# Performance work log

Measured on AMD Instinct MI355X. Metric: run time of the kernel, lower is better.

Reference implementation:

```python
import jax, jax.numpy as jnp
import numpy as np

N = 50000      # nodes
E = 800000     # edges (before self-loops)
G = 128        # graphs in batch
IN = 128       # input_dim
H = 4          # heads
D = 32         # hidden_dim per head (H*D = 128)
L = 3          # n_layers
COND = 7       # data.stats features
LAT = 32       # latent_dim
NEG_SLOPE = 0.2


def setup_inputs() -> dict:
    key = jax.random.key(0)
    ks = jax.random.split(key, 10)
    s = 0.1
    return {
        "x": jax.random.normal(ks[0], (N, IN), jnp.float32),
        "cond": jax.random.normal(ks[1], (G, COND), jnp.float32),
        "W": jax.random.normal(ks[2], (L, IN, H * D), jnp.float32) * s,
        "a_src": jax.random.normal(ks[3], (L, H, D), jnp.float32) * s,
        "a_dst": jax.random.normal(ks[4], (L, H, D), jnp.float32) * s,
        "conv_bias": jnp.zeros((L, H * D), jnp.float32),
        "bn_gamma": jnp.ones((H * D + COND,), jnp.float32),
        "bn_beta": jnp.zeros((H * D + COND,), jnp.float32),
        "fc_w": jax.random.normal(ks[5], (H * D + COND, LAT), jnp.float32) * s,
        "fc_b": jnp.zeros((LAT,), jnp.float32),
        "edge_index": jax.random.randint(ks[6], (2, E), 0, N, jnp.int32),
        "batch": jnp.sort(jax.random.randint(ks[7], (N,), 0, G, jnp.int32)),
    }


def _leaky(x, slope):
    return jnp.where(x > 0, x, slope * x)


def _gat_layer(x, W, a_s, a_d, b, src, dst):
    # x: [N, F_in] -> h: [N, H, D]
    h = (x @ W).reshape(N, H, D)
    al_s = jnp.einsum("nhd,hd->nh", h, a_s)   # [N, H]
    al_d = jnp.einsum("nhd,hd->nh", h, a_d)   # [N, H]
    e = _leaky(al_s[src] + al_d[dst], NEG_SLOPE)          # [Etot, H]
    m = jax.ops.segment_max(e, dst, num_segments=N)       # per-dst max
    ex = jnp.exp(e - m[dst])
    denom = jax.ops.segment_sum(ex, dst, num_segments=N)  # [N, H]
    alpha = ex / (denom[dst] + 1e-16)                     # softmax over in-edges
    out = jax.ops.segment_sum(alpha[:, :, None] * h[src], dst, num_segments=N)
    return out.reshape(N, H * D) + b


def reference(x, cond, W, a_src, a_dst, conv_bias, bn_gamma, bn_beta, fc_w, fc_b,
              edge_index, batch):
    loops = jnp.arange(N, dtype=edge_index.dtype)  # PyG GATConv adds self-loops
    src = jnp.concatenate([edge_index[0], loops])
    dst = jnp.concatenate([edge_index[1], loops])
    for i in range(L):
        x = _gat_layer(x, W[i], a_src[i], a_dst[i], conv_bias[i], src, dst)
        x = _leaky(x, 0.2)  # encoder's LeakyReLU(0.2); dropout skipped (eval)
    pooled = jax.ops.segment_sum(x, batch, num_segments=G)  # global_add_pool
    out = jnp.concatenate([pooled, cond], axis=1)           # [G, H*D+7]
    mu = out.mean(axis=0)
    var = out.var(axis=0)                                   # biased, as torch BN
    out = (out - mu) / jnp.sqrt(var + 1e-5) * bn_gamma + bn_beta
    return out @ fc_w + fc_b                                # [G, LAT]
```

## Files before the change

### kernel.cpp

```cpp
#include <hip/hip_runtime.h>
#include <math.h>

#define N_NODES 50000
#define N_EDGES 800000
#define ETOT (N_EDGES + N_NODES)
#define G_GRAPHS 128
#define HD 128
#define COND_F 7
#define NFEAT 135
#define LAT 32
#define L_LAYERS 3
#define SLOPE 0.2f
#define MAXDEG 96

typedef __attribute__((ext_vector_type(8))) short bf16x8;
typedef __attribute__((ext_vector_type(4))) float f32x4;

__device__ __forceinline__ float leaky_(float x) { return x > 0.f ? x : SLOPE * x; }

__device__ __forceinline__ unsigned short f2bf_(float f) {
    unsigned int u = __float_as_uint(f);
    u += 0x7FFF + ((u >> 16) & 1);
    return (unsigned short)(u >> 16);
}
__device__ __forceinline__ float bf2f_(unsigned short b) {
    return __uint_as_float((unsigned int)b << 16);
}
__device__ __forceinline__ unsigned int pack_bf2_(float lo, float hi) {
    unsigned int ulo = __float_as_uint(lo); ulo += 0x7FFF + ((ulo >> 16) & 1);
    unsigned int uhi = __float_as_uint(hi); uhi += 0x7FFF + ((uhi >> 16) & 1);
    return (ulo >> 16) | (uhi & 0xFFFF0000u);
}

__global__ void scatter_kernel(const int* __restrict__ ei, int* __restrict__ fill,
                               int* __restrict__ csr) {
    int i = blockIdx.x * blockDim.x + threadIdx.x;
    if (i >= ETOT) return;
    int srcv, dstv;
    if (i < N_EDGES) { srcv = ei[i]; dstv = ei[N_EDGES + i]; }
    else { srcv = dstv = i - N_EDGES; }
    int slot = atomicAdd(&fill[dstv], 1);
    if (slot < MAXDEG) csr[slot * N_NODES + dstv] = srcv;
}

__global__ void prep_kernel(const float* __restrict__ W, const float* __restrict__ a_s,
                            const float* __restrict__ a_d, unsigned short* __restrict__ Wt,
                            unsigned short* __restrict__ Wa) {
    int i = blockIdx.x * blockDim.x + threadIdx.x;
    const int NW = L_LAYERS * 128 * 128;
    if (i < NW) {
        int l = i >> 14, rem = i & 16383, k = rem >> 7, n = rem & 127;
        unsigned int u = __float_as_uint(W[i]);
        u += 0x7FFF + ((u >> 16) & 1);
        Wt[(l << 14) + n * 128 + k] = (unsigned short)(u >> 16);
        return;
    }
    int j = i - NW;
    if (j >= L_LAYERS * 16 * 128) return;
    int l = j >> 11, rem = j & 2047, c = rem >> 7, k = rem & 127;
    float v = 0.f;
    if (c < 8) {
        int h = c >> 1;
        const float* av = (c & 1) ? &a_d[l * 128 + h * 32] : &a_s[l * 128 + h * 32];
        const float* wrow = &W[(l << 14) + k * 128 + h * 32];
#pragma unroll
        for (int d = 0; d < 32; ++d) v = fmaf(wrow[d], av[d], v);
    }
    Wa[j] = f2bf_(v);
}

__global__ __launch_bounds__(256) void gemm_mfma_kernel(
    const float* __restrict__ x, const unsigned short* __restrict__ Wt,
    const unsigned short* __restrict__ Wa,
    unsigned short* __restrict__ h_bf, float* __restrict__ al_s,
    float* __restrict__ al_d) {
    __shared__ __align__(16) unsigned short xs[64 * 128];
    int t = threadIdx.x;
    int lane = t & 63;
    int w = t >> 6;
    int row0 = blockIdx.x * 64;

    {
        int r = t >> 2, c0 = (t & 3) * 32;
        int gr = row0 + r;
        unsigned int upk[16];
        if (gr < N_NODES) {
            const float* src = &x[(size_t)gr * 128 + c0];
#pragma unroll
            for (int i = 0; i < 8; ++i) {
                float4 v = *(const float4*)&src[i * 4];
                upk[i * 2 + 0] = pack_bf2_(v.x, v.y);
                upk[i * 2 + 1] = pack_bf2_(v.z, v.w);
            }
        } else {
#pragma unroll
            for (int i = 0; i < 16; ++i) upk[i] = 0;
        }
        char* base = (char*)xs + r * 256;
#pragma unroll
        for (int i = 0; i < 4; ++i) {
            int cb = c0 * 2 + i * 16;
            int sw = cb ^ ((r & 7) << 4);
            *(uint4*)(base + sw) = make_uint4(upk[i * 4 + 0], upk[i * 4 + 1],
                                              upk[i * 4 + 2], upk[i * 4 + 3]);
        }
    }
    int l15 = lane & 15, g16 = lane >> 4;
    int cn = w * 32;
    bf16x8 bfr[2][4];
#pragma unroll
    for (int ct = 0; ct < 2; ++ct)
#pragma unroll
        for (int ks = 0; ks < 4; ++ks)
            bfr[ct][ks] = *(const bf16x8*)&Wt[(size_t)(cn + ct * 16 + l15) * 128 + ks * 32 + g16 * 8];
    bf16x8 bfrL[4];
    if (w == 0) {
#pragma unroll
        for (int ks = 0; ks < 4; ++ks)
            bfrL[ks] = *(const bf16x8*)&Wa[l15 * 128 + ks * 32 + g16 * 8];
    }
    __syncthreads();

    f32x4 acc[4][2];
    f32x4 accL[4];
#pragma unroll
    for (int rt = 0; rt < 4; ++rt) {
#pragma unroll
        for (int ct = 0; ct < 2; ++ct) acc[rt][ct] = (f32x4){0.f, 0.f, 0.f, 0.f};
        accL[rt] = (f32x4){0.f, 0.f, 0.f, 0.f};
    }

#pragma unroll
    for (int ks = 0; ks < 4; ++ks) {
        bf16x8 af[4];
#pragma unroll
        for (int rt = 0; rt < 4; ++rt) {
            int r = rt * 16 + l15;
            int cb = ks * 64 + g16 * 16;
            af[rt] = *(const bf16x8*)((const char*)xs + r * 256 + (cb ^ ((r & 7) << 4)));
        }
#pragma unroll
        for (int rt = 0; rt < 4; ++rt)
#pragma unroll
            for (int ct = 0; ct < 2; ++ct)
                acc[rt][ct] = __builtin_amdgcn_mfma_f32_16x16x32_bf16(
                    af[rt], bfr[ct][ks], acc[rt][ct], 0, 0, 0);
        if (w == 0) {
#pragma unroll
            for (int rt = 0; rt < 4; ++rt)
                accL[rt] = __builtin_amdgcn_mfma_f32_16x16x32_bf16(
                    af[rt], bfrL[ks], accL[rt], 0, 0, 0);
        }
    }

    __syncthreads();

#pragma unroll
    for (int rt = 0; rt < 4; ++rt) {
#pragma unroll
        for (int j = 0; j < 4; ++j) {
            int r = rt * 16 + g16 * 4 + j;
            int sw = (r & 7) << 4;
            char* rowb = (char*)xs + r * 256;
            *(unsigned short*)(rowb + (((cn + l15) * 2) ^ sw)) = f2bf_(acc[rt][0][j]);
            *(unsigned short*)(rowb + (((cn + 16 + l15) * 2) ^ sw)) = f2bf_(acc[rt][1][j]);
        }
    }
    if (w == 0) {
#pragma unroll
        for (int rt = 0; rt < 4; ++rt) {
#pragma unroll
            for (int j = 0; j < 4; ++j) {
                int grow = row0 + rt * 16 + g16 * 4 + j;
                if (l15 < 8 && grow < N_NODES) {
                    float v = accL[rt][j];
                    if (l15 & 1) al_d[grow * 4 + (l15 >> 1)] = v;
                    else al_s[grow * 4 + (l15 >> 1)] = v;
                }
            }
        }
    }
    __syncthreads();
#pragma unroll
    for (int i = 0; i < 4; ++i) {
        int flat = i * 4096 + t * 16;
        int r = flat >> 8;
        int cb = flat & 255;
        uint4 v = *(const uint4*)((const char*)xs + r * 256 + (cb ^ ((r & 7) << 4)));
        int gr = row0 + r;
        if (gr < N_NODES)
            *(uint4*)((char*)&h_bf[(size_t)gr * 128] + cb) = v;
    }
}

__global__ __launch_bounds__(256) void agg_kernel(
    const unsigned short* __restrict__ h_bf, const float* __restrict__ al_s,
    const float* __restrict__ al_d, const int* __restrict__ deg_arr,
    const int* __restrict__ csr, const float* __restrict__ bias,
    float* __restrict__ xout) {
    __shared__ float alph[4][64][4];
    __shared__ int srcs[4][64];
    __shared__ float bounce[4][160];
    int wslot = threadIdx.x >> 6;
    int wv = (blockIdx.x * blockDim.x + threadIdx.x) >> 6;
    int lane = threadIdx.x & 63;
    if (wv >= N_NODES) return;
    int node = wv;
    int deg = deg_arr[node];
    float4 ad = *(const float4*)&al_d[node * 4];

    if (deg <= 64) {
        float e0 = -1e30f, e1 = -1e30f, e2 = -1e30f, e3 = -1e30f;
        int s_l = 0;
        if (lane < deg) {
            s_l = csr[lane * N_NODES + node];
            float4 as = *(const float4*)&al_s[s_l * 4];
            e0 = leaky_(as.x + ad.x);
            e1 = leaky_(as.y + ad.y);
            e2 = leaky_(as.z + ad.z);
            e3 = leaky_(as.w + ad.w);
        }
        float m0 = e0, m1 = e1, m2 = e2, m3 = e3;
#pragma unroll
        for (int off = 1; off < 64; off <<= 1) {
            m0 = fmaxf(m0, __shfl_xor(m0, off));
            m1 = fmaxf(m1, __shfl_xor(m1, off));
            m2 = fmaxf(m2, __shfl_xor(m2, off));
            m3 = fmaxf(m3, __shfl_xor(m3, off));
        }
        float x0 = 0.f, x1 = 0.f, x2 = 0.f, x3 = 0.f;
        if (lane < deg) {
            x0 = __expf(e0 - m0);
            x1 = __expf(e1 - m1);
            x2 = __expf(e2 - m2);
            x3 = __expf(e3 - m3);
        }
        float d0 = x0, d1 = x1, d2 = x2, d3 = x3;
#pragma unroll
        for (int off = 1; off < 64; off <<= 1) {
            d0 += __shfl_xor(d0, off);
            d1 += __shfl_xor(d1, off);
            d2 += __shfl_xor(d2, off);
            d3 += __shfl_xor(d3, off);
        }
        float i0 = 1.f / (d0 + 1e-16f), i1 = 1.f / (d1 + 1e-16f);
        float i2 = 1.f / (d2 + 1e-16f), i3 = 1.f / (d3 + 1e-16f);

        *(float4*)&alph[wslot][lane][0] =
            make_float4(x0 * i0, x1 * i1, x2 * i2, x3 * i3);
        srcs[wslot][lane] = s_l;

        int grp = lane >> 4, li = lane & 15;
        int hq = li >> 2;
        float facc[8];
#pragma unroll
        for (int k = 0; k < 8; ++k) facc[k] = 0.f;
        int degr = (deg + 3) & ~3;
        int j0 = 0;
        for (; j0 + 8 <= degr; j0 += 8) {
            int eA = j0 + grp, eB = j0 + 4 + grp;
            int sA = srcs[wslot][eA];
            int sB = srcs[wslot][eB];
            float aA = alph[wslot][eA][hq];
            float aB = alph[wslot][eB][hq];
            uint4 vA = *(const uint4*)&h_bf[(size_t)sA * 128 + li * 8];
            uint4 vB = *(const uint4*)&h_bf[(size_t)sB * 128 + li * 8];
            facc[0] = fmaf(aA, __uint_as_float(vA.x << 16), facc[0]);
            facc[1] = fmaf(aA, __uint_as_float(vA.x & 0xFFFF0000u), facc[1]);
            facc[2] = fmaf(aA, __uint_as_float(vA.y << 16), facc[2]);
            facc[3] = fmaf(aA, __uint_as_float(vA.y & 0xFFFF0000u), facc[3]);
            facc[4] = fmaf(aA, __uint_as_float(vA.z << 16), facc[4]);
            facc[5] = fmaf(aA, __uint_as_float(vA.z & 0xFFFF0000u), facc[5]);
            facc[6] = fmaf(aA, __uint_as_float(vA.w << 16), facc[6]);
            facc[7] = fmaf(aA, __uint_as_float(vA.w & 0xFFFF0000u), facc[7]);
            facc[0] = fmaf(aB, __uint_as_float(vB.x << 16), facc[0]);
            facc[1] = fmaf(aB, __uint_as_float(vB.x & 0xFFFF0000u), facc[1]);
            facc[2] = fmaf(aB, __uint_as_float(vB.y << 16), facc[2]);
            facc[3] = fmaf(aB, __uint_as_float(vB.y & 0xFFFF0000u), facc[3]);
            facc[4] = fmaf(aB, __uint_as_float(vB.z << 16), facc[4]);
            facc[5] = fmaf(aB, __uint_as_float(vB.z & 0xFFFF0000u), facc[5]);
            facc[6] = fmaf(aB, __uint_as_float(vB.w << 16), facc[6]);
            facc[7] = fmaf(aB, __uint_as_float(vB.w & 0xFFFF0000u), facc[7]);
        }
        if (j0 < degr) {
            int e = j0 + grp;
            int s = srcs[wslot][e];
            float a = alph[wslot][e][hq];
            uint4 v = *(const uint4*)&h_bf[(size_t)s * 128 + li * 8];
            facc[0] = fmaf(a, __uint_as_float(v.x << 16), facc[0]);
            facc[1] = fmaf(a, __uint_as_float(v.x & 0xFFFF0000u), facc[1]);
            facc[2] = fmaf(a, __uint_as_float(v.y << 16), facc[2]);
            facc[3] = fmaf(a, __uint_as_float(v.y & 0xFFFF0000u), facc[3]);
            facc[4] = fmaf(a, __uint_as_float(v.z << 16), facc[4]);
            facc[5] = fmaf(a, __uint_as_float(v.z & 0xFFFF0000u), facc[5]);
            facc[6] = fmaf(a, __uint_as_float(v.w << 16), facc[6]);
            facc[7] = fmaf(a, __uint_as_float(v.w & 0xFFFF0000u), facc[7]);
        }
#pragma unroll
        for (int k = 0; k < 8; ++k) {
            facc[k] += __shfl_xor(facc[k], 16);
            facc[k] += __shfl_xor(facc[k], 32);
        }
        if (grp == 0) {
#pragma unroll
            for (int k = 0; k < 8; ++k) bounce[wslot][k * 17 + li] = facc[k];
        }
        int fA = lane, fB = lane + 64;
        float o0 = bounce[wslot][(fA & 7) * 17 + (fA >> 3)];
        float o1 = bounce[wslot][(fB & 7) * 17 + (fB >> 3)];
        xout[node * 128 + fA] = leaky_(o0 + bias[fA]);
        xout[node * 128 + fB] = leaky_(o1 + bias[fB]);
    } else {
        int f0 = lane, f1 = lane + 64;
        int hA = lane >> 5;
        float acc0 = 0.f, acc1 = 0.f;
        float m0 = -1e30f, m1 = -1e30f, m2 = -1e30f, m3 = -1e30f;
        for (int e = lane; e < deg; e += 64) {
            int s = csr[e * N_NODES + node];
            float4 as = *(const float4*)&al_s[s * 4];
            m0 = fmaxf(m0, leaky_(as.x + ad.x));
            m1 = fmaxf(m1, leaky_(as.y + ad.y));
            m2 = fmaxf(m2, leaky_(as.z + ad.z));
            m3 = fmaxf(m3, leaky_(as.w + ad.w));
        }
#pragma unroll
        for (int off = 1; off < 64; off <<= 1) {
            m0 = fmaxf(m0, __shfl_xor(m0, off));
            m1 = fmaxf(m1, __shfl_xor(m1, off));
            m2 = fmaxf(m2, __shfl_xor(m2, off));
            m3 = fmaxf(m3, __shfl_xor(m3, off));
        }
        float d0 = 0.f, d1 = 0.f, d2 = 0.f, d3 = 0.f;
        for (int e = lane; e < deg; e += 64) {
            int s = csr[e * N_NODES + node];
            float4 as = *(const float4*)&al_s[s * 4];
            d0 += __expf(leaky_(as.x + ad.x) - m0);
            d1 += __expf(leaky_(as.y + ad.y) - m1);
            d2 += __expf(leaky_(as.z + ad.z) - m2);
            d3 += __expf(leaky_(as.w + ad.w) - m3);
        }
#pragma unroll
        for (int off = 1; off < 64; off <<= 1) {
            d0 += __shfl_xor(d0, off);
            d1 += __shfl_xor(d1, off);
            d2 += __shfl_xor(d2, off);
            d3 += __shfl_xor(d3, off);
        }
        float i0 = 1.f / (d0 + 1e-16f), i1 = 1.f / (d1 + 1e-16f);
        float i2 = 1.f / (d2 + 1e-16f), i3 = 1.f / (d3 + 1e-16f);
        float adA = hA ? ad.y : ad.x, adB = hA ? ad.w : ad.z;
        float mA = hA ? m1 : m0, mB = hA ? m3 : m2;
        float iA = hA ? i1 : i0, iB = hA ? i3 : i2;
        for (int e = 0; e < deg; ++e) {
            int s = csr[e * N_NODES + node];
            float asA = al_s[s * 4 + hA];
            float asB = al_s[s * 4 + 2 + hA];
            float aA = __expf(leaky_(asA + adA) - mA) * iA;
            float aB = __expf(leaky_(asB + adB) - mB) * iB;
            acc0 = fmaf(aA, bf2f_(h_bf[s * 128 + f0]), acc0);
            acc1 = fmaf(aB, bf2f_(h_bf[s * 128 + f1]), acc1);
        }
        xout[node * 128 + f0] = leaky_(acc0 + bias[f0]);
        xout[node * 128 + f1] = leaky_(acc1 + bias[f1]);
    }
}

#define POOL_CHUNK 128
__global__ __launch_bounds__(256) void pool_kernel(const float* __restrict__ x,
                                                   const int* __restrict__ batch,
                                                   float* __restrict__ pooled) {
    int wv = (blockIdx.x * blockDim.x + threadIdx.x) >> 6;
    int lane = threadIdx.x & 63;
    int n0 = wv * POOL_CHUNK;
    if (n0 >= N_NODES) return;
    int n1 = min(n0 + POOL_CHUNK, N_NODES);
    float a0 = 0.f, a1 = 0.f;
    int gcur = batch[n0];
    for (int n = n0; n < n1; ++n) {
        int g = batch[n];
        if (g != gcur) {
            atomicAdd(&pooled[gcur * 128 + lane], a0);
            atomicAdd(&pooled[gcur * 128 + 64 + lane], a1);
            a0 = a1 = 0.f;
            gcur = g;
        }
        a0 += x[n * 128 + lane];
        a1 += x[n * 128 + 64 + lane];
    }
    atomicAdd(&pooled[gcur * 128 + lane], a0);
    atomicAdd(&pooled[gcur * 128 + 64 + lane], a1);
}

__global__ __launch_bounds__(256) void bnfc_kernel(
    const float* __restrict__ pooled, const float* __restrict__ cond,
    const float* __restrict__ gamma, const float* __restrict__ beta,
    const float* __restrict__ fcw, const float* __restrict__ fcb,
    float* __restrict__ out) {
    __shared__ float Y[G_GRAPHS * NFEAT];
    __shared__ float scale[NFEAT], shift[NFEAT];
    int t = threadIdx.x;
    for (int idx = t; idx < G_GRAPHS * NFEAT; idx += 256) {
        int g = idx / NFEAT, f = idx % NFEAT;
        Y[idx] = (f < HD) ? pooled[g * HD + f] : cond[g * COND_F + (f - HD)];
    }
    __syncthreads();
    if (t < NFEAT) {
        float s = 0.f;
        for (int g = 0; g < G_GRAPHS; ++g) s += Y[g * NFEAT + t];
        float mean = s * (1.f / G_GRAPHS);
        float v = 0.f;
        for (int g = 0; g < G_GRAPHS; ++g) {
            float dd = Y[g * NFEAT + t] - mean;
            v += dd * dd;
        }
        v *= (1.f / G_GRAPHS);
        float inv = rsqrtf(v + 1e-5f);
        float sc = gamma[t] * inv;
        scale[t] = sc;
        shift[t] = beta[t] - mean * sc;
    }
    __syncthreads();
    for (int idx = t; idx < G_GRAPHS * NFEAT; idx += 256) {
        int f = idx % NFEAT;
        Y[idx] = Y[idx] * scale[f] + shift[f];
    }
    __syncthreads();
    for (int idx = t; idx < G_GRAPHS * LAT; idx += 256) {
        int g = idx >> 5, j = idx & 31;
        float acc = fcb[j];
        for (int f = 0; f < NFEAT; ++f) acc = fmaf(Y[g * NFEAT + f], fcw[f * LAT + j], acc);
        out[idx] = acc;
    }
}

extern "C" void kernel_launch(void* const* d_in, const int* in_sizes, int n_in,
                              void* d_out, int out_size, void* d_ws, size_t ws_size,
                              hipStream_t stream) {
    const float* x_in = (const float*)d_in[0];
    const float* cond = (const float*)d_in[1];
    const float* W = (const float*)d_in[2];
    const float* a_src = (const float*)d_in[3];
    const float* a_dst = (const float*)d_in[4];
    const float* conv_bias = (const float*)d_in[5];
    const float* bn_gamma = (const float*)d_in[6];
    const float* bn_beta = (const float*)d_in[7];
    const float* fc_w = (const float*)d_in[8];
    const float* fc_b = (const float*)d_in[9];
    const int* edge_index = (const int*)d_in[10];
    const int* batch = (const int*)d_in[11];
    float* out = (float*)d_out;

    char* ws = (char*)d_ws;
    size_t off = 0;
    auto alloc = [&](size_t bytes) {
        void* p = ws + off;
        off += (bytes + 255) & ~(size_t)255;
        return p;
    };
    float* bufP = (float*)alloc((size_t)N_NODES * 128 * 4);
    unsigned short* h_bf = (unsigned short*)alloc((size_t)N_NODES * 128 * 2);
    unsigned short* Wt = (unsigned short*)alloc((size_t)L_LAYERS * 128 * 128 * 2);
    unsigned short* Wa = (unsigned short*)alloc((size_t)L_LAYERS * 16 * 128 * 2);
    float* als = (float*)alloc((size_t)N_NODES * 4 * 4);
    float* ald = (float*)alloc((size_t)N_NODES * 4 * 4);
    float* pooled = (float*)alloc((size_t)G_GRAPHS * HD * 4);
    int* fill = (int*)alloc((size_t)N_NODES * 4);
    int* csr = (int*)alloc((size_t)N_NODES * MAXDEG * 4);

    hipMemsetAsync(fill, 0, N_NODES * 4, stream);
    hipMemsetAsync(pooled, 0, G_GRAPHS * HD * 4, stream);
    const int NPREP = L_LAYERS * 128 * 128 + L_LAYERS * 16 * 128;
    prep_kernel<<<(NPREP + 255) / 256, 256, 0, stream>>>(W, a_src, a_dst, Wt, Wa);
    scatter_kernel<<<(ETOT + 255) / 256, 256, 0, stream>>>(edge_index, fill, csr);

    const float* xcur = x_in;
    for (int l = 0; l < L_LAYERS; ++l) {
        gemm_mfma_kernel<<<(N_NODES + 63) / 64, 256, 0, stream>>>(
            xcur, Wt + (size_t)l * 128 * 128, Wa + (size_t)l * 16 * 128,
            h_bf, als, ald);
        agg_kernel<<<N_NODES / 4, 256, 0, stream>>>(
            h_bf, als, ald, fill, csr, conv_bias + l * 128, bufP);
        xcur = bufP;
    }

    int pool_waves = (N_NODES + POOL_CHUNK - 1) / POOL_CHUNK;
    pool_kernel<<<(pool_waves + 3) / 4, 256, 0, stream>>>(xcur, batch, pooled);
    bnfc_kernel<<<1, 256, 0, stream>>>(pooled, cond, bn_gamma, bn_beta, fc_w, fc_b, out);
}
```

Baseline: 314.5 us.

## Partition CSR build by destination range with shared-memory counters

Replaces the global-atomic edge scatter with 64 blocks that each own a slice of destination nodes. Each block scans the full dst array and counts into shared-memory atomics, writing self-loops first, then writes the clamped counts to fill, which removes the memset. This trades global atomic contention for every block reading all 800K dst indices, and uses only 64 blocks on a GPU with many more CUs. Self-loops now always sit at slot 0, so the order of edges within each node's list changes.

```diff
diff --git a/kernel.cpp b/kernel.cpp
--- a/kernel.cpp
+++ b/kernel.cpp
@@ -12,6 +12,8 @@
 #define L_LAYERS 3
 #define SLOPE 0.2f
 #define MAXDEG 96
+#define SC_BLOCKS 64
+#define SC_RANGE ((N_NODES + SC_BLOCKS - 1) / SC_BLOCKS)
 
 typedef __attribute__((ext_vector_type(8))) short bf16x8;
 typedef __attribute__((ext_vector_type(4))) float f32x4;
@@ -32,15 +34,43 @@
     return (ulo >> 16) | (uhi & 0xFFFF0000u);
 }
 
-__global__ void scatter_kernel(const int* __restrict__ ei, int* __restrict__ fill,
-                               int* __restrict__ csr) {
-    int i = blockIdx.x * blockDim.x + threadIdx.x;
-    if (i >= ETOT) return;
-    int srcv, dstv;
-    if (i < N_EDGES) { srcv = ei[i]; dstv = ei[N_EDGES + i]; }
-    else { srcv = dstv = i - N_EDGES; }
-    int slot = atomicAdd(&fill[dstv], 1);
-    if (slot < MAXDEG) csr[slot * N_NODES + dstv] = srcv;
+__global__ __launch_bounds__(1024) void scatter_kernel(const int* __restrict__ ei,
+                                                       int* __restrict__ fill,
+                                                       int* __restrict__ csr) {
+    __shared__ int cnt[SC_RANGE];
+    int b = blockIdx.x, t = threadIdx.x;
+    int base = b * SC_RANGE;
+    int lim = min(SC_RANGE, N_NODES - base);
+    for (int j = t; j < lim; j += 1024) {
+        cnt[j] = 1;
+        csr[base + j] = base + j;
+    }
+    __syncthreads();
+    const int4* d4 = (const int4*)(ei + N_EDGES);
+    const int nv = N_EDGES / 4;
+    int up = base + lim;
+    for (int i = t; i < nv; i += 1024) {
+        int4 d = d4[i];
+        int idx = i * 4;
+        if (d.x >= base && d.x < up) {
+            int slot = atomicAdd(&cnt[d.x - base], 1);
+            if (slot < MAXDEG) csr[slot * N_NODES + d.x] = ei[idx + 0];
+        }
+        if (d.y >= base && d.y < up) {
+            int slot = atomicAdd(&cnt[d.y - base], 1);
+            if (slot < MAXDEG) csr[slot * N_NODES + d.y] = ei[idx + 1];
+        }
+        if (d.z >= base && d.z < up) {
+            int slot = atomicAdd(&cnt[d.z - base], 1);
+            if (slot < MAXDEG) csr[slot * N_NODES + d.z] = ei[idx + 2];
+        }
+        if (d.w >= base && d.w < up) {
+            int slot = atomicAdd(&cnt[d.w - base], 1);
+            if (slot < MAXDEG) csr[slot * N_NODES + d.w] = ei[idx + 3];
+        }
+    }
+    __syncthreads();
+    for (int j = t; j < lim; j += 1024) fill[base + j] = min(cnt[j], MAXDEG);
 }
 
 __global__ void prep_kernel(const float* __restrict__ W, const float* __restrict__ a_s,
@@ -467,11 +497,10 @@
     int* fill = (int*)alloc((size_t)N_NODES * 4);
     int* csr = (int*)alloc((size_t)N_NODES * MAXDEG * 4);
 
-    hipMemsetAsync(fill, 0, N_NODES * 4, stream);
     hipMemsetAsync(pooled, 0, G_GRAPHS * HD * 4, stream);
     const int NPREP = L_LAYERS * 128 * 128 + L_LAYERS * 16 * 128;
     prep_kernel<<<(NPREP + 255) / 256, 256, 0, stream>>>(W, a_src, a_dst, Wt, Wa);
-    scatter_kernel<<<(ETOT + 255) / 256, 256, 0, stream>>>(edge_index, fill, csr);
+    scatter_kernel<<<SC_BLOCKS, 1024, 0, stream>>>(edge_index, fill, csr);
 
     const float* xcur = x_in;
     for (int l = 0; l < L_LAYERS; ++l) {
```

Measured after the change: 480.8 us. +52.9%, slower.
